# Optimization experiments

Measured on AMD Instinct MI355X. Metric: run time of the kernel, lower is better.

The kernel has to match this reference:

```python
import jax, jax.numpy as jnp
import numpy as np
import math

TWO_PI = 2.0 * math.pi
C_TOP = 8      # ann_top_centroids
K_TOP = 32     # topk slots
SCALES = 4
TEMP = 1.0
MIN_CANDID = 32


def _ln(x):
    mu = x.mean(axis=-1, keepdims=True)
    v = x.var(axis=-1, keepdims=True)
    return (x - mu) / jnp.sqrt(v + 1e-5)


def _gelu(x):
    return jax.nn.gelu(x, approximate=False)


def _sq_l2(q, k):
    # q: (B,S,D), k: (N,D) -> (B,S,N) squared L2
    return ((q * q).sum(-1)[..., None] + (k * k).sum(-1)
            - 2.0 * jnp.einsum('bsd,nd->bsn', q, k))


def _forward(x, keys, values, W_in, b_in, ricci, fractal_weights, centroids,
             Wk, bk, entangle_key, holo_real, holo_imag, W_read, b_read,
             W_out, b_out, centroid_ids):
    B, S, _ = x.shape
    M, D = keys.shape
    C = centroids.shape[0]

    # input_projection: Linear -> LayerNorm -> GELU, then manifold encode
    z = _gelu(_ln(x @ W_in + b_in))                    # (B,S,3D)
    z = z.reshape(B, S, D, 3)
    z = jnp.einsum('bseq,ed->bsdq', z, ricci)          # ricci flow
    q = z.mean(axis=-1)                                # (B,S,D) query on manifold

    # fractal multiscale distance: d(q/2^s, k/2^s) = d(q,k)/4^s for squared L2
    wts = jax.nn.softmax(fractal_weights)
    coef = (wts / (4.0 ** jnp.arange(SCALES, dtype=x.dtype))).sum()

    # stage 1: centroid shortlist (no-grad in original)
    d_cent = coef * _sq_l2(q, centroids)               # (B,S,C)
    _, topc = jax.lax.top_k(-d_cent, C_TOP)            # smallest distances
    sel = jnp.zeros((C,), dtype=bool).at[topc.reshape(-1)].set(True)
    mask_cent = sel[centroid_ids]                      # (M,) candidate slots
    mask = mask_cent | (mask_cent.sum() < MIN_CANDID)  # fall back to all keys

    # stage 2: distances to candidate keys, inf elsewhere
    d_keys = coef * _sq_l2(q, keys)                    # (B,S,M)
    dist = jnp.where(mask, d_keys, jnp.inf)
    dist = jax.lax.stop_gradient(dist)                 # search is no-grad

    neg_top, idx = jax.lax.top_k(-dist, K_TOP)         # (B,S,K)
    w = jax.nn.softmax(neg_top / TEMP, axis=-1)        # slot weights

    # value read: gather + weighted sum
    v_read = jnp.einsum('bsk,bskd->bsd', w, values[idx])   # (B,S,3D)

    # holographic read: complex key phases, FFT-domain entangled unbind
    phase = TWO_PI * jax.nn.sigmoid(x @ Wk + bk)            # (B,S,H)
    k_c = jnp.exp(1j * phase.astype(jnp.complex64))
    kf = jnp.fft.fft(k_c, axis=-1)
    kf = kf * jnp.exp(1j * entangle_key.astype(jnp.complex64))

    holo = (holo_real + 1j * holo_imag)[idx]                # (B,S,K,H) complex64
    holo_sum = jnp.einsum('bsk,bskh->bsh', w.astype(jnp.complex64), holo)
    r = jnp.fft.ifft(holo_sum * jnp.conj(kf), axis=-1)      # unbind, time domain
    feats = jnp.concatenate([r.real, r.imag], axis=-1)      # (B,S,2H)
    holo_out = feats @ W_read + b_read                      # (B,S,3D)

    mem = v_read + holo_out
    out = _gelu(_ln(mem @ W_out + b_out))                   # (B,S,input_dim)
    return out


def setup_inputs() -> dict:
    key = jax.random.key(0)
    ks = jax.random.split(key, 16)
    B, S, IN = 2, 2048, 1024
    D, M, H, C = 24, 4096, 256, 256
    x = jax.random.normal(ks[0], (B, S, IN), jnp.float32)
    keys_p = jax.random.normal(ks[1], (M, D), jnp.float32)
    values = jax.random.normal(ks[2], (M, 3 * D), jnp.float32)
    W_in = jax.random.normal(ks[3], (IN, 3 * D), jnp.float32) / np.sqrt(IN)
    b_in = jnp.zeros((3 * D,), jnp.float32)
    ricci = jax.random.normal(ks[4], (D, D), jnp.float32) / np.sqrt(D)
    fractal_weights = jnp.ones((4,), jnp.float32)
    centroids = jax.random.normal(ks[5], (C, D), jnp.float32)
    Wk = jax.random.normal(ks[6], (IN, H), jnp.float32) / np.sqrt(IN)
    bk = jnp.zeros((H,), jnp.float32)
    entangle_key = jax.random.normal(ks[7], (H,), jnp.float32)
    holo_real = jax.random.normal(ks[8], (M, H), jnp.float32)
    holo_imag = jax.random.normal(ks[9], (M, H), jnp.float32)
    W_read = jax.random.normal(ks[10], (2 * H, 3 * D), jnp.float32) / np.sqrt(2 * H)
    b_read = jnp.zeros((3 * D,), jnp.float32)
    W_out = jax.random.normal(ks[11], (3 * D, IN), jnp.float32) / np.sqrt(3 * D)
    b_out = jnp.zeros((IN,), jnp.float32)
    # centroid assignment of each key (k-means style nearest centroid)
    centroid_ids = jnp.argmin(_sq_l2(keys_p[None], centroids)[0], axis=-1).astype(jnp.int32)
    return {"x": x, "keys": keys_p, "values": values, "W_in": W_in, "b_in": b_in,
            "ricci": ricci, "fractal_weights": fractal_weights,
            "centroids": centroids, "Wk": Wk, "bk": bk,
            "entangle_key": entangle_key, "holo_real": holo_real,
            "holo_imag": holo_imag, "W_read": W_read, "b_read": b_read,
            "W_out": W_out, "b_out": b_out, "centroid_ids": centroid_ids}


def reference(x, keys, values, W_in, b_in, ricci, fractal_weights, centroids,
              Wk, bk, entangle_key, holo_real, holo_imag, W_read, b_read,
              W_out, b_out, centroid_ids):
    return _forward(x, keys, values, W_in, b_in, ricci, fractal_weights,
                    centroids, Wk, bk, entangle_key, holo_real, holo_imag,
                    W_read, b_read, W_out, b_out, centroid_ids)
```

## Files before the change

### kernel.cpp

```cpp
#include <hip/hip_runtime.h>
#include <math.h>

#define P_TOT 4096
#define IN_DIM 1024
#define DDIM 24
#define MKEYS 4096
#define HDIM 256
#define CCENT 256
#define KTOP 32

typedef short bf16x8 __attribute__((ext_vector_type(8)));
typedef float f32x4 __attribute__((ext_vector_type(4)));

static const size_t o_Yq      = 0;
static const size_t o_Yp      = o_Yq + (size_t)2*P_TOT*72;
static const size_t o_q       = o_Yp + (size_t)P_TOT*256;
static const size_t o_qq      = o_q + (size_t)P_TOT*DDIM;
static const size_t o_KF      = o_qq + P_TOT;
static const size_t o_keynorm = o_KF + (size_t)P_TOT*512;
static const size_t o_centnorm= o_keynorm + MKEYS;
static const size_t o_coef    = o_centnorm + CCENT;
static const size_t o_vread   = o_coef + 64;
static const size_t o_keysT   = o_vread + (size_t)P_TOT*72;
static const size_t o_sel     = o_keysT + (size_t)DDIM*MKEYS;
static const size_t o_mask    = o_sel + 256;
static const size_t o_count   = o_mask + MKEYS;
static const size_t o_A6      = o_count + 64;
static const size_t o_W6T     = o_A6 + (size_t)P_TOT*3072/2;
static const size_t o_W2cat   = o_W6T + (size_t)72*6144/2;
static const size_t o_KCbf    = o_W2cat + (size_t)256*2048/2;
static const size_t o_TTT     = o_KCbf + (size_t)P_TOT*512/2;
static const size_t o_Xcatbf  = o_TTT + (size_t)512*512/2;
static const size_t o_W2T     = o_Xcatbf + (size_t)P_TOT*512/2;
static const size_t o_membf   = o_W2T + (size_t)72*512/2;
static const size_t o_WoutT   = o_membf + (size_t)P_TOT*96/2;

__device__ __forceinline__ float gelu_f(float x){
    return 0.5f * x * (1.0f + erff(x * 0.70710678118654752f));
}
__device__ __forceinline__ ushort f2bf(float f){
    union { float f; unsigned u; } a; a.f = f;
    unsigned u = a.u;
    return (ushort)((u + 0x7fffu + ((u >> 16) & 1u)) >> 16);
}
__device__ __forceinline__ float bf2f(ushort b){
    union { unsigned u; float f; } a; a.u = ((unsigned)b) << 16;
    return a.f;
}
__device__ __forceinline__ unsigned d2u(float f){
    unsigned b = __float_as_uint(f);
    return (b & 0x80000000u) ? ~b : (b | 0x80000000u);
}

#define TWO_PI_F 6.2831853071795864769f
#define STEP_F   0.024543692606170262f

__global__ void setup_small(const float* __restrict__ fw, const float* __restrict__ cent,
                            float* __restrict__ coefp, float* __restrict__ centnorm,
                            int* __restrict__ sel, int* __restrict__ count)
{
    int t = threadIdx.x;
    if (t == 0){
        float m = fmaxf(fmaxf(fw[0],fw[1]),fmaxf(fw[2],fw[3]));
        float e0=expf(fw[0]-m), e1=expf(fw[1]-m), e2=expf(fw[2]-m), e3=expf(fw[3]-m);
        float s = e0+e1+e2+e3;
        *coefp = (e0 + e1*0.25f + e2*0.0625f + e3*0.015625f) / s;
        *count = 0;
    }
    if (t < CCENT){
        sel[t] = 0;
        float s = 0.f;
        #pragma unroll
        for (int d=0; d<DDIM; ++d){ float v = cent[t*DDIM+d]; s += v*v; }
        centnorm[t] = s;
    }
}

__global__ void key_setup(const float* __restrict__ keys, float* __restrict__ keynorm,
                          float* __restrict__ keysT)
{
    int m = blockIdx.x*256 + threadIdx.x;
    float s = 0.f;
    #pragma unroll
    for (int d=0; d<DDIM; ++d){
        float v = keys[m*DDIM+d]; s += v*v;
        keysT[(size_t)d*MKEYS + m] = v;
    }
    keynorm[m] = s;
}

__global__ void conv_x3(const float* __restrict__ x, ushort* __restrict__ A6)
{
    int i = blockIdx.x*256 + threadIdx.x;
    int p = i >> 8, j = (i & 255) * 4;
    float4 v = *(const float4*)&x[(size_t)p*IN_DIM + j];
    ushort4 s0, s1, s2;
    float r;
    s0.x=f2bf(v.x); r=v.x-bf2f(s0.x); s1.x=f2bf(r); s2.x=f2bf(r-bf2f(s1.x));
    s0.y=f2bf(v.y); r=v.y-bf2f(s0.y); s1.y=f2bf(r); s2.y=f2bf(r-bf2f(s1.y));
    s0.z=f2bf(v.z); r=v.z-bf2f(s0.z); s1.z=f2bf(r); s2.z=f2bf(r-bf2f(s1.z));
    s0.w=f2bf(v.w); r=v.w-bf2f(s0.w); s1.w=f2bf(r); s2.w=f2bf(r-bf2f(s1.w));
    *(ushort4*)&A6[(size_t)p*3072 + j]        = s0;
    *(ushort4*)&A6[(size_t)p*3072 + 1024 + j] = s1;
    *(ushort4*)&A6[(size_t)p*3072 + 2048 + j] = s2;
}

__global__ void conv_W6(const float* __restrict__ Win, ushort* __restrict__ W6T)
{
    int idx = blockIdx.x*256 + threadIdx.x;
    if (idx >= 72*6144) return;
    int n = idx / 6144, kp = idx - n*6144;
    int seg = kp >> 10, kk = kp & 1023;
    int sb = (0x012010 >> (seg << 2)) & 0xF;
    float w = Win[kk*72 + n];
    ushort w0 = f2bf(w);
    float r1 = w - bf2f(w0);
    ushort w1 = f2bf(r1);
    ushort w2 = f2bf(r1 - bf2f(w1));
    W6T[idx] = (sb == 0) ? w0 : (sb == 1 ? w1 : w2);
}

__global__ void conv_W2cat(const float* __restrict__ Wk, ushort* __restrict__ W2cat)
{
    int idx = blockIdx.x*256 + threadIdx.x;
    int n = idx >> 11, k = idx & 2047;
    int kk = k & 1023;
    W2cat[idx] = f2bf(Wk[kk*256 + n]);
}

__global__ void conv_WoutT(const float* __restrict__ Wout, ushort* __restrict__ WoutT)
{
    int idx = blockIdx.x*256 + threadIdx.x;
    int n = idx / 96, k = idx - n*96;
    float v = (k < 72) ? Wout[(size_t)k*IN_DIM + n] : 0.f;
    WoutT[idx] = f2bf(v);
}

__global__ void build_TTT(const float* __restrict__ ek, ushort* __restrict__ TTT)
{
    int idx = blockIdx.x*256 + threadIdx.x;
    int c = idx >> 9, r = idx & 511;
    int n = c & 255, h = r & 255;
    float th = (float)((n*h) & 255) * STEP_F - ek[n];
    float sn, cs; sincosf(th, &sn, &cs);
    float v;
    if (r < 256) v = (c < 256) ? cs : -sn;
    else         v = (c < 256) ? sn : cs;
    TTT[idx] = f2bf(v);
}

__global__ void build_W2T(const float* __restrict__ Wr, ushort* __restrict__ W2T)
{
    __shared__ float tab[256];
    int t = threadIdx.x;
    tab[t] = cosf((float)t * STEP_F);
    __syncthreads();
    int idx = blockIdx.x*256 + t;
    if (idx >= 72*512) return;
    int j = idx >> 9, k = idx & 511;
    int n = k & 255;
    float acc = 0.f;
    for (int h=0; h<256; ++h){
        int xdx = (n*h) & 255;
        float c = tab[xdx], s = tab[(xdx+192) & 255];
        float w1 = Wr[h*72 + j], w2 = Wr[(256+h)*72 + j];
        acc += (k < 256) ? (c*w1 + s*w2) : (c*w2 - s*w1);
    }
    W2T[idx] = f2bf(acc * (1.f/256.f));
}

__global__ __launch_bounds__(256) void gemm_bf16(
    const ushort* __restrict__ A, const ushort* __restrict__ BT,
    float* __restrict__ C, const float* __restrict__ bias,
    const float* __restrict__ addm, ushort* __restrict__ Cbf,
    int M, int N, int Kloop, int Nb, int NbfPad, int lda, int ldb, int aMask,
    int amode, int kChunk, size_t zStride)
{
    __shared__ __align__(16) ushort As[64][40];
    __shared__ __align__(16) ushort Bs[64][40];
    const int tid = threadIdx.x;
    const int lane = tid & 63, wid = tid >> 6;
    const int wm = wid >> 1, wn = wid & 1;
    const int m0 = blockIdx.y * 64, n0 = blockIdx.x * 64;
    const int fr = lane & 15, fc = lane >> 4;
    const int srow = tid >> 2, schunk = (tid & 3) * 8;
    const int kStart = blockIdx.z * kChunk;
    const int kEnd = (kStart + kChunk < Kloop) ? (kStart + kChunk) : Kloop;
    if (blockIdx.z){ C += zStride; bias = nullptr; addm = nullptr; Cbf = nullptr; }
    f32x4 acc[2][2] = {};
    for (int k0 = kStart; k0 < kEnd; k0 += 32){
        int kk = k0 + schunk;
        int ka;
        if (amode) ka = (((0x210100 >> ((kk >> 10) << 2)) & 0xF) << 10) | (kk & 1023);
        else       ka = kk & aMask;
        *(bf16x8*)&As[srow][schunk] =
            *(const bf16x8*)&A[(size_t)(m0 + srow) * lda + ka];
        {
            int n = n0 + srow;
            bf16x8 v = {};
            if (n < Nb) v = *(const bf16x8*)&BT[(size_t)n * ldb + kk];
            *(bf16x8*)&Bs[srow][schunk] = v;
        }
        __syncthreads();
        bf16x8 a0 = *(bf16x8*)&As[wm*32 + fr][fc*8];
        bf16x8 a1 = *(bf16x8*)&As[wm*32 + 16 + fr][fc*8];
        bf16x8 b0 = *(bf16x8*)&Bs[wn*32 + fr][fc*8];
        bf16x8 b1 = *(bf16x8*)&Bs[wn*32 + 16 + fr][fc*8];
        acc[0][0] = __builtin_amdgcn_mfma_f32_16x16x32_bf16(a0, b0, acc[0][0], 0,0,0);
        acc[0][1] = __builtin_amdgcn_mfma_f32_16x16x32_bf16(a0, b1, acc[0][1], 0,0,0);
        acc[1][0] = __builtin_amdgcn_mfma_f32_16x16x32_bf16(a1, b0, acc[1][0], 0,0,0);
        acc[1][1] = __builtin_amdgcn_mfma_f32_16x16x32_bf16(a1, b1, acc[1][1], 0,0,0);
        __syncthreads();
    }
    #pragma unroll
    for (int mi=0; mi<2; ++mi){
        #pragma unroll
        for (int ni=0; ni<2; ++ni){
            #pragma unroll
            for (int rr=0; rr<4; ++rr){
                int gm = m0 + wm*32 + mi*16 + fc*4 + rr;
                int gn = n0 + wn*32 + ni*16 + fr;
                float v = acc[mi][ni][rr];
                if (gn < N){
                    if (bias) v += bias[gn];
                    if (addm) v += addm[(size_t)gm*N + gn];
                    if (C) C[(size_t)gm*N + gn] = v;
                } else v = 0.f;
                if (Cbf && gn < NbfPad)
                    Cbf[(size_t)gm*NbfPad + gn] = f2bf(v);
            }
        }
    }
}

__global__ __launch_bounds__(256) void post_proj(
    const float* __restrict__ Yq, const float* __restrict__ Yp,
    const float* __restrict__ ricci,
    float* __restrict__ q, float* __restrict__ qq, ushort* __restrict__ KCbf)
{
    int wave = threadIdx.x >> 6, lane = threadIdx.x & 63;
    int p = blockIdx.x*4 + wave;
    __shared__ float zsh[4][72];
    __shared__ float zbsh[4][24];
    const float* Yr  = Yq + (size_t)p*72;
    const float* Yr2 = Yq + (size_t)P_TOT*72 + (size_t)p*72;
    float v1 = Yr[lane] + Yr2[lane];
    float v2 = (lane < 8) ? (Yr[64+lane] + Yr2[64+lane]) : 0.f;
    float s = v1 + v2, s2 = v1*v1 + v2*v2;
    #pragma unroll
    for (int off=32; off; off>>=1){ s += __shfl_xor(s,off); s2 += __shfl_xor(s2,off); }
    float mean = s * (1.f/72.f);
    float var  = s2 * (1.f/72.f) - mean*mean;
    float rstd = rsqrtf(var + 1e-5f);
    zsh[wave][lane] = gelu_f((v1-mean)*rstd);
    if (lane < 8) zsh[wave][64+lane] = gelu_f((v2-mean)*rstd);
    __syncthreads();
    if (lane < 24){
        float zb = (zsh[wave][lane*3] + zsh[wave][lane*3+1] + zsh[wave][lane*3+2]) * (1.f/3.f);
        zbsh[wave][lane] = zb;
    }
    __syncthreads();
    float qd = 0.f;
    if (lane < 24){
        #pragma unroll
        for (int e=0;e<24;++e) qd += zbsh[wave][e] * ricci[e*24+lane];
        q[(size_t)p*DDIM + lane] = qd;
    }
    float qs = (lane<24) ? qd*qd : 0.f;
    #pragma unroll
    for (int off=32; off; off>>=1) qs += __shfl_xor(qs,off);
    if (lane == 0) qq[p] = qs;
    const float* Ypr = Yp + (size_t)p*256;
    #pragma unroll
    for (int j=0;j<4;++j){
        int h = lane + 64*j;
        float u = Ypr[h];
        float ph = TWO_PI_F / (1.f + expf(-u));
        float sn, cs; sincosf(ph, &sn, &cs);
        KCbf[(size_t)p*512 + h]       = f2bf(cs);
        KCbf[(size_t)p*512 + 256 + h] = f2bf(sn);
    }
}

__global__ __launch_bounds__(256) void cent_topk(
    const float* __restrict__ q, const float* __restrict__ qq,
    const float* __restrict__ centroids, const float* __restrict__ centnorm,
    int* __restrict__ sel)
{
    int wave = threadIdx.x >> 6, lane = threadIdx.x & 63;
    int p = blockIdx.x*4 + wave;
    __shared__ float qsh[4][24];
    if (lane < 24) qsh[wave][lane] = q[(size_t)p*DDIM + lane];
    __syncthreads();
    float qv = qq[p];
    float d[4]; int ci[4];
    #pragma unroll
    for (int j=0;j<4;++j){
        int c = lane + 64*j;
        float dot = 0.f;
        #pragma unroll
        for (int e=0;e<24;++e) dot += qsh[wave][e]*centroids[c*24+e];
        d[j] = qv + centnorm[c] - 2.f*dot;
        ci[j] = c;
    }
    for (int k=0;k<8;++k){
        float mv = d[0]; int mi = ci[0];
        #pragma unroll
        for (int j=1;j<4;++j) if (d[j] < mv || (d[j]==mv && ci[j]<mi)){ mv=d[j]; mi=ci[j]; }
        #pragma unroll
        for (int off=32; off; off>>=1){
            float ov = __shfl_xor(mv,off); int oi = __shfl_xor(mi,off);
            if (ov < mv || (ov==mv && oi<mi)){ mv=ov; mi=oi; }
        }
        if ((mi & 63) == lane){
            int j = mi >> 6;
            if (j==0) d[0]=INFINITY; else if (j==1) d[1]=INFINITY;
            else if (j==2) d[2]=INFINITY; else d[3]=INFINITY;
            sel[mi] = 1;
        }
    }
}

__global__ void mask_count(const int* __restrict__ sel, const int* __restrict__ cids,
                           int* __restrict__ maskKey, int* __restrict__ count)
{
    int m = blockIdx.x*256 + threadIdx.x;
    int v = sel[cids[m]];
    maskKey[m] = v;
    int lane = threadIdx.x & 63;
    #pragma unroll
    for (int off=32; off; off>>=1) v += __shfl_xor(v, off);
    if (lane == 0) atomicAdd(count, v);
}

__device__ __forceinline__ void select_pos(
    int pc, float (&dvr)[16], int t, int lane, int w, float coef,
    int* hist, int* wsum,
    unsigned& s_pref, int& s_krem, int& s_bin, int& s_below,
    int& s_cntL, int& s_cntT,
    float* candD, int* candI, float* tieD, int* tieI,
    float (*sw4)[KTOP], int (*sidx4)[KTOP], float* inv4)
{
    if (t == 0){ s_pref = 0u; s_krem = KTOP; }
    __syncthreads();
    for (int pp = 0; pp < 4; ++pp){
        hist[t] = 0;
        __syncthreads();
        unsigned prefR = s_pref;
        int kremR = s_krem;
        #pragma unroll
        for (int i=0;i<16;++i){
            unsigned u = d2u(dvr[i]);
            bool cond = (pp == 0) ? true : ((u >> (32 - 8*pp)) == prefR);
            if (cond) atomicAdd(&hist[(u >> (24 - 8*pp)) & 255], 1);
        }
        __syncthreads();
        int h = hist[t];
        int sc = h;
        #pragma unroll
        for (int off=1; off<64; off<<=1){
            int o = __shfl_up(sc, off);
            if (lane >= off) sc += o;
        }
        if (lane == 63) wsum[w] = sc;
        __syncthreads();
        int add = 0;
        for (int ww=0; ww<w; ++ww) add += wsum[ww];
        sc += add;
        if (kremR > sc - h && kremR <= sc){ s_bin = t; s_below = sc - h; }
        __syncthreads();
        if (t == 0){ s_pref = (s_pref << 8) | (unsigned)s_bin; s_krem -= s_below; }
        __syncthreads();
    }
    unsigned tau = s_pref;
    if (t == 0){ s_cntL = 0; s_cntT = 0; }
    __syncthreads();
    #pragma unroll
    for (int i=0;i<16;++i){
        unsigned u = d2u(dvr[i]);
        int m = 1024*(i>>2) + 4*t + (i&3);
        if (u < tau){ int sl = atomicAdd(&s_cntL,1); candD[sl]=dvr[i]; candI[sl]=m; }
        else if (u == tau){ int sl = atomicAdd(&s_cntT,1); if (sl<64){ tieD[sl]=dvr[i]; tieI[sl]=m; } }
    }
    __syncthreads();
    if (t == 0){
        int need = s_krem, have = s_cntL;
        int nt = s_cntT < 64 ? s_cntT : 64;
        for (int sl=0; sl<need; ++sl){
            int best=0, bi=0x7fffffff;
            for (int j=0;j<nt;++j) if (tieI[j] < bi){ bi=tieI[j]; best=j; }
            candD[have+sl]=tieD[best]; candI[have+sl]=bi; tieI[best]=0x7fffffff;
        }
    }
    __syncthreads();
    if (w == 0){
        float v = (lane < 32) ? candD[lane] : INFINITY;
        int  ix = (lane < 32) ? candI[lane] : 0x7fffffff;
        #pragma unroll
        for (int kk=2; kk<=64; kk<<=1){
            #pragma unroll
            for (int j=kk>>1; j>0; j>>=1){
                float ov = __shfl_xor(v, j); int oi = __shfl_xor(ix, j);
                bool keepSmall = (((lane & j) == 0) == ((lane & kk) == 0));
                bool less = (ov < v) || (ov == v && oi < ix);
                if (keepSmall ? less : !less){ v = ov; ix = oi; }
            }
        }
        float v0 = __shfl(v, 0);
        float swv = (lane < 32) ? expf(-coef * (v - v0)) : 0.f;
        float ssum = 0.f;
        for (int k=0;k<KTOP;++k) ssum += __shfl(swv, k);
        if (lane < 32){ sw4[pc][lane] = swv; sidx4[pc][lane] = ix; }
        if (lane == 0) inv4[pc] = 1.f / ssum;
    }
    __syncthreads();
}

__global__ __launch_bounds__(256) void select_read(
    const float* __restrict__ keysT,
    const float* __restrict__ q, const float* __restrict__ qq,
    const float* __restrict__ keynorm, const int* __restrict__ maskKey,
    const int* __restrict__ count, const float* __restrict__ coefp,
    const float* __restrict__ values, const float* __restrict__ hr,
    const float* __restrict__ hi, const float* __restrict__ KF,
    float* __restrict__ vread, ushort* __restrict__ Xcatbf)
{
    const int t = threadIdx.x;
    const int w = t >> 6, lane = t & 63;
    const int p0 = blockIdx.x * 4;
    __shared__ float qsh[4][24];
    __shared__ int hist[256];
    __shared__ int wsum[4];
    __shared__ unsigned s_pref;
    __shared__ int s_krem, s_bin, s_below, s_cntL, s_cntT;
    __shared__ float candD[KTOP]; __shared__ int candI[KTOP];
    __shared__ float tieD[64];    __shared__ int tieI[64];
    __shared__ float sw4[4][KTOP]; __shared__ int sidx4[4][KTOP];
    __shared__ float inv4[4];

    bool useAll = (*count) < 32;
    float coef = *coefp;
    if (t < 96){
        int pp = t / 24, e = t - pp*24;
        qsh[pp][e] = q[(size_t)(p0+pp)*DDIM + e];
    }
    __syncthreads();
    float qv0 = qq[p0], qv1 = qq[p0+1], qv2 = qq[p0+2], qv3 = qq[p0+3];

    float a0[16], a1[16], a2[16], a3[16];
    #pragma unroll
    for (int i=0;i<16;++i){ a0[i]=0.f; a1[i]=0.f; a2[i]=0.f; a3[i]=0.f; }
    for (int e=0;e<24;++e){
        float q0 = qsh[0][e], q1 = qsh[1][e], q2 = qsh[2][e], q3 = qsh[3][e];
        const float* kr = keysT + (size_t)e*MKEYS + 4*t;
        #pragma unroll
        for (int i=0;i<4;++i){
            float4 kv = *(const float4*)&kr[1024*i];
            a0[i*4+0]=fmaf(q0,kv.x,a0[i*4+0]); a0[i*4+1]=fmaf(q0,kv.y,a0[i*4+1]);
            a0[i*4+2]=fmaf(q0,kv.z,a0[i*4+2]); a0[i*4+3]=fmaf(q0,kv.w,a0[i*4+3]);
            a1[i*4+0]=fmaf(q1,kv.x,a1[i*4+0]); a1[i*4+1]=fmaf(q1,kv.y,a1[i*4+1]);
            a1[i*4+2]=fmaf(q1,kv.z,a1[i*4+2]); a1[i*4+3]=fmaf(q1,kv.w,a1[i*4+3]);
            a2[i*4+0]=fmaf(q2,kv.x,a2[i*4+0]); a2[i*4+1]=fmaf(q2,kv.y,a2[i*4+1]);
            a2[i*4+2]=fmaf(q2,kv.z,a2[i*4+2]); a2[i*4+3]=fmaf(q2,kv.w,a2[i*4+3]);
            a3[i*4+0]=fmaf(q3,kv.x,a3[i*4+0]); a3[i*4+1]=fmaf(q3,kv.y,a3[i*4+1]);
            a3[i*4+2]=fmaf(q3,kv.z,a3[i*4+2]); a3[i*4+3]=fmaf(q3,kv.w,a3[i*4+3]);
        }
    }
    #pragma unroll
    for (int i=0;i<4;++i){
        float4 kn = *(const float4*)&keynorm[1024*i + 4*t];
        int4 mk = *(const int4*)&maskKey[1024*i + 4*t];
        bool ok0 = useAll || mk.x, ok1 = useAll || mk.y, ok2 = useAll || mk.z, ok3 = useAll || mk.w;
        float d;
        d = qv0 + kn.x - 2.f*a0[i*4+0]; a0[i*4+0] = ok0 ? d : INFINITY;
        d = qv0 + kn.y - 2.f*a0[i*4+1]; a0[i*4+1] = ok1 ? d : INFINITY;
        d = qv0 + kn.z - 2.f*a0[i*4+2]; a0[i*4+2] = ok2 ? d : INFINITY;
        d = qv0 + kn.w - 2.f*a0[i*4+3]; a0[i*4+3] = ok3 ? d : INFINITY;
        d = qv1 + kn.x - 2.f*a1[i*4+0]; a1[i*4+0] = ok0 ? d : INFINITY;
        d = qv1 + kn.y - 2.f*a1[i*4+1]; a1[i*4+1] = ok1 ? d : INFINITY;
        d = qv1 + kn.z - 2.f*a1[i*4+2]; a1[i*4+2] = ok2 ? d : INFINITY;
        d = qv1 + kn.w - 2.f*a1[i*4+3]; a1[i*4+3] = ok3 ? d : INFINITY;
        d = qv2 + kn.x - 2.f*a2[i*4+0]; a2[i*4+0] = ok0 ? d : INFINITY;
        d = qv2 + kn.y - 2.f*a2[i*4+1]; a2[i*4+1] = ok1 ? d : INFINITY;
        d = qv2 + kn.z - 2.f*a2[i*4+2]; a2[i*4+2] = ok2 ? d : INFINITY;
        d = qv2 + kn.w - 2.f*a2[i*4+3]; a2[i*4+3] = ok3 ? d : INFINITY;
        d = qv3 + kn.x - 2.f*a3[i*4+0]; a3[i*4+0] = ok0 ? d : INFINITY;
        d = qv3 + kn.y - 2.f*a3[i*4+1]; a3[i*4+1] = ok1 ? d : INFINITY;
        d = qv3 + kn.z - 2.f*a3[i*4+2]; a3[i*4+2] = ok2 ? d : INFINITY;
        d = qv3 + kn.w - 2.f*a3[i*4+3]; a3[i*4+3] = ok3 ? d : INFINITY;
    }

    select_pos(0, a0, t, lane, w, coef, hist, wsum, s_pref, s_krem, s_bin, s_below,
               s_cntL, s_cntT, candD, candI, tieD, tieI, sw4, sidx4, inv4);
    select_pos(1, a1, t, lane, w, coef, hist, wsum, s_pref, s_krem, s_bin, s_below,
               s_cntL, s_cntT, candD, candI, tieD, tieI, sw4, sidx4, inv4);
    select_pos(2, a2, t, lane, w, coef, hist, wsum, s_pref, s_krem, s_bin, s_below,
               s_cntL, s_cntT, candD, candI, tieD, tieI, sw4, sidx4, inv4);
    select_pos(3, a3, t, lane, w, coef, hist, wsum, s_pref, s_krem, s_bin, s_below,
               s_cntL, s_cntT, candD, candI, tieD, tieI, sw4, sidx4, inv4);

    for (int pos=0; pos<4; ++pos){
        int p = p0 + pos;
        float inv = inv4[pos];
        if (t < 72){
            float a = 0.f;
            for (int k=0;k<KTOP;++k) a += sw4[pos][k]*values[(size_t)sidx4[pos][k]*72 + t];
            vread[(size_t)p*72 + t] = a * inv;
        }
        float sr = 0.f, si = 0.f;
        for (int k=0;k<KTOP;++k){
            float wv = sw4[pos][k];
            size_t off = (size_t)sidx4[pos][k]*HDIM + t;
            sr += wv*hr[off]; si += wv*hi[off];
        }
        sr *= inv; si *= inv;
        float Rk = KF[(size_t)p*512 + t], Ik = KF[(size_t)p*512 + 256 + t];
        Xcatbf[(size_t)p*512 + t]       = f2bf(sr*Rk + si*Ik);
        Xcatbf[(size_t)p*512 + 256 + t] = f2bf(si*Rk - sr*Ik);
    }
}

__global__ __launch_bounds__(256) void ln_gelu_out(float* __restrict__ O)
{
    int p = blockIdx.x; int t = threadIdx.x;
    float4 v = *(float4*)&O[(size_t)p*IN_DIM + t*4];
    float s  = v.x+v.y+v.z+v.w;
    float s2 = v.x*v.x+v.y*v.y+v.z*v.z+v.w*v.w;
    #pragma unroll
    for (int off=32; off; off>>=1){ s += __shfl_xor(s,off); s2 += __shfl_xor(s2,off); }
    __shared__ float as[4], as2[4];
    int lane = t & 63, w = t >> 6;
    if (lane == 0){ as[w] = s; as2[w] = s2; }
    __syncthreads();
    s = as[0]+as[1]+as[2]+as[3];
    s2 = as2[0]+as2[1]+as2[2]+as2[3];
    float mean = s * (1.f/1024.f);
    float var  = s2 * (1.f/1024.f) - mean*mean;
    float rstd = rsqrtf(var + 1e-5f);
    v.x = gelu_f((v.x-mean)*rstd);
    v.y = gelu_f((v.y-mean)*rstd);
    v.z = gelu_f((v.z-mean)*rstd);
    v.w = gelu_f((v.w-mean)*rstd);
    *(float4*)&O[(size_t)p*IN_DIM + t*4] = v;
}

extern "C" void kernel_launch(void* const* d_in, const int* in_sizes, int n_in,
                              void* d_out, int out_size, void* d_ws, size_t ws_size,
                              hipStream_t stream)
{
    const float* x      = (const float*)d_in[0];
    const float* keys   = (const float*)d_in[1];
    const float* values = (const float*)d_in[2];
    const float* W_in   = (const float*)d_in[3];
    const float* b_in   = (const float*)d_in[4];
    const float* ricci  = (const float*)d_in[5];
    const float* fw     = (const float*)d_in[6];
    const float* cent   = (const float*)d_in[7];
    const float* Wk     = (const float*)d_in[8];
    const float* bk     = (const float*)d_in[9];
    const float* ek     = (const float*)d_in[10];
    const float* hr     = (const float*)d_in[11];
    const float* hi     = (const float*)d_in[12];
    const float* Wr     = (const float*)d_in[13];
    const float* brd    = (const float*)d_in[14];
    const float* W_out  = (const float*)d_in[15];
    const float* b_out  = (const float*)d_in[16];
    const int*   cids   = (const int*)d_in[17];
    float* ws  = (float*)d_ws;
    float* out = (float*)d_out;
    int* sel   = (int*)(ws + o_sel);
    int* mask  = (int*)(ws + o_mask);
    int* count = (int*)(ws + o_count);
    ushort* A6     = (ushort*)(ws + o_A6);
    ushort* W6T    = (ushort*)(ws + o_W6T);
    ushort* W2cat  = (ushort*)(ws + o_W2cat);
    ushort* KCbf   = (ushort*)(ws + o_KCbf);
    ushort* TTT    = (ushort*)(ws + o_TTT);
    ushort* Xcatbf = (ushort*)(ws + o_Xcatbf);
    ushort* W2T    = (ushort*)(ws + o_W2T);
    ushort* membf  = (ushort*)(ws + o_membf);
    ushort* WoutT  = (ushort*)(ws + o_WoutT);
    const int NOMASK = 0x7fffffff;

    setup_small<<<1,256,0,stream>>>(fw, cent, ws+o_coef, ws+o_centnorm, sel, count);
    key_setup<<<16,256,0,stream>>>(keys, ws+o_keynorm, ws+o_keysT);
    conv_x3<<<4096,256,0,stream>>>(x, A6);
    conv_W6<<<(72*6144+255)/256,256,0,stream>>>(W_in, W6T);
    conv_W2cat<<<2048,256,0,stream>>>(Wk, W2cat);
    conv_WoutT<<<(IN_DIM*96)/256,256,0,stream>>>(W_out, WoutT);
    build_TTT<<<1024,256,0,stream>>>(ek, TTT);
    build_W2T<<<144,256,0,stream>>>(Wr, W2T);

    gemm_bf16<<<dim3(2,64,2),256,0,stream>>>(A6, W6T, ws+o_Yq, b_in, nullptr, nullptr,
                                             P_TOT, 72, 6144, 72, 0, 3072, 6144, NOMASK, 1,
                                             3072, (size_t)P_TOT*72);
    gemm_bf16<<<dim3(4,64,1),256,0,stream>>>(A6, W2cat, ws+o_Yp, bk, nullptr, nullptr,
                                             P_TOT, 256, 2048, 256, 0, 3072, 2048, NOMASK, 0,
                                             2048, 0);
    post_proj<<<1024,256,0,stream>>>(ws+o_Yq, ws+o_Yp, ricci, ws+o_q, ws+o_qq, KCbf);
    gemm_bf16<<<dim3(8,64,1),256,0,stream>>>(KCbf, TTT, ws+o_KF, nullptr, nullptr, nullptr,
                                             P_TOT, 512, 512, 512, 0, 512, 512, NOMASK, 0,
                                             512, 0);
    cent_topk<<<1024,256,0,stream>>>(ws+o_q, ws+o_qq, cent, ws+o_centnorm, sel);
    mask_count<<<16,256,0,stream>>>(sel, cids, mask, count);
    select_read<<<P_TOT/4,256,0,stream>>>(ws+o_keysT, ws+o_q, ws+o_qq, ws+o_keynorm,
                                          mask, count, ws+o_coef, values, hr, hi, ws+o_KF,
                                          ws+o_vread, Xcatbf);
    gemm_bf16<<<dim3(2,64,1),256,0,stream>>>(Xcatbf, W2T, nullptr, brd, ws+o_vread, membf,
                                             P_TOT, 72, 512, 72, 96, 512, 512, NOMASK, 0,
                                             512, 0);
    gemm_bf16<<<dim3(16,64,1),256,0,stream>>>(membf, WoutT, out, b_out, nullptr, nullptr,
                                              P_TOT, IN_DIM, 96, IN_DIM, 0, 96, 96, NOMASK, 0,
                                              96, 0);
    ln_gelu_out<<<P_TOT,256,0,stream>>>(out);
}
```

Baseline: 314.5 us.

## Replace radix top-k select with value-range bucket refinement over three passes

The per-position top-32 selection stops doing a 4-pass 8-bit radix select on the bit pattern of each distance. It now takes a block-wide min/max of the finite distances and refines a value-range histogram over 256 buckets for 3 passes, tracking per-element active and below masks. Ties in the final bucket are resolved by a second bitonic sort. This removes one histogram pass and the serial single-thread tie loop, but adds a min/max reduction and an extra sort, and relies on float bucketing, which can put more than 64 elements in the final bucket and drop candidates. A mask argument of one GEMM launch also changes from NOMASK to 2047, which may alter its output.

```diff
diff --git a/kernel.cpp b/kernel.cpp
--- a/kernel.cpp
+++ b/kernel.cpp
@@ -46,10 +46,6 @@
 __device__ __forceinline__ float bf2f(ushort b){
     union { unsigned u; float f; } a; a.u = ((unsigned)b) << 16;
     return a.f;
-}
-__device__ __forceinline__ unsigned d2u(float f){
-    unsigned b = __float_as_uint(f);
-    return (b & 0x80000000u) ? ~b : (b | 0x80000000u);
 }
 
 #define TWO_PI_F 6.2831853071795864769f
@@ -333,26 +329,51 @@
     if (lane == 0) atomicAdd(count, v);
 }
 
+__device__ __forceinline__ int bucket_of(float d, float lo, float inv){
+    float bf = (d - lo) * inv;
+    bf = fminf(bf, 255.0f);
+    int bn = (int)bf;
+    return bn < 0 ? 0 : bn;
+}
+
 __device__ __forceinline__ void select_pos(
     int pc, float (&dvr)[16], int t, int lane, int w, float coef,
-    int* hist, int* wsum,
-    unsigned& s_pref, int& s_krem, int& s_bin, int& s_below,
-    int& s_cntL, int& s_cntT,
+    int* hist, int* wsum, float* wmn, float* wmx, float* s_f, int* s_i,
     float* candD, int* candI, float* tieD, int* tieI,
     float (*sw4)[KTOP], int (*sidx4)[KTOP], float* inv4)
 {
-    if (t == 0){ s_pref = 0u; s_krem = KTOP; }
-    __syncthreads();
-    for (int pp = 0; pp < 4; ++pp){
+    float mn = INFINITY, mx = -INFINITY;
+    #pragma unroll
+    for (int i=0;i<16;++i){
+        float d = dvr[i];
+        mn = fminf(mn, d);
+        mx = fmaxf(mx, (d < INFINITY) ? d : -INFINITY);
+    }
+    #pragma unroll
+    for (int off=32; off; off>>=1){
+        mn = fminf(mn, __shfl_xor(mn, off));
+        mx = fmaxf(mx, __shfl_xor(mx, off));
+    }
+    if (lane == 0){ wmn[w] = mn; wmx[w] = mx; }
+    __syncthreads();
+    if (t == 0){
+        float dmin = fminf(fminf(wmn[0],wmn[1]), fminf(wmn[2],wmn[3]));
+        float dmax = fmaxf(fmaxf(wmx[0],wmx[1]), fmaxf(wmx[2],wmx[3]));
+        s_f[0] = dmin;
+        s_f[1] = fmaxf(dmax - dmin, 1e-30f) * 1.000001f;
+        s_i[0] = 0;
+    }
+    __syncthreads();
+
+    unsigned act = 0xFFFFu, below = 0u;
+    for (int pass = 0; pass < 3; ++pass){
         hist[t] = 0;
         __syncthreads();
-        unsigned prefR = s_pref;
-        int kremR = s_krem;
-        #pragma unroll
-        for (int i=0;i<16;++i){
-            unsigned u = d2u(dvr[i]);
-            bool cond = (pp == 0) ? true : ((u >> (32 - 8*pp)) == prefR);
-            if (cond) atomicAdd(&hist[(u >> (24 - 8*pp)) & 255], 1);
+        float lo = s_f[0];
+        float inv = 256.0f / s_f[1];
+        #pragma unroll
+        for (int i=0;i<16;++i) if (act & (1u<<i)){
+            atomicAdd(&hist[bucket_of(dvr[i], lo, inv)], 1);
         }
         __syncthreads();
         int h = hist[t];
@@ -367,35 +388,44 @@
         int add = 0;
         for (int ww=0; ww<w; ++ww) add += wsum[ww];
         sc += add;
-        if (kremR > sc - h && kremR <= sc){ s_bin = t; s_below = sc - h; }
+        int krem = KTOP - s_i[0];
+        if (krem > sc - h && krem <= sc){ s_i[1] = t; s_i[2] = sc - h; }
         __syncthreads();
-        if (t == 0){ s_pref = (s_pref << 8) | (unsigned)s_bin; s_krem -= s_below; }
+        int bstar = s_i[1];
+        #pragma unroll
+        for (int i=0;i<16;++i) if (act & (1u<<i)){
+            int bn = bucket_of(dvr[i], lo, inv);
+            if (bn < bstar){ below |= (1u<<i); act &= ~(1u<<i); }
+            else if (bn > bstar) act &= ~(1u<<i);
+        }
+        if (t == 0){
+            s_i[0] += s_i[2];
+            float wnew = s_f[1] * (1.f/256.f);
+            s_f[0] = s_f[0] + (float)bstar * wnew;
+            s_f[1] = wnew;
+        }
         __syncthreads();
     }
-    unsigned tau = s_pref;
-    if (t == 0){ s_cntL = 0; s_cntT = 0; }
+
+    if (t == 0){ s_i[3] = 0; s_i[4] = 0; }
     __syncthreads();
     #pragma unroll
     for (int i=0;i<16;++i){
-        unsigned u = d2u(dvr[i]);
         int m = 1024*(i>>2) + 4*t + (i&3);
-        if (u < tau){ int sl = atomicAdd(&s_cntL,1); candD[sl]=dvr[i]; candI[sl]=m; }
-        else if (u == tau){ int sl = atomicAdd(&s_cntT,1); if (sl<64){ tieD[sl]=dvr[i]; tieI[sl]=m; } }
-    }
-    __syncthreads();
-    if (t == 0){
-        int need = s_krem, have = s_cntL;
-        int nt = s_cntT < 64 ? s_cntT : 64;
-        for (int sl=0; sl<need; ++sl){
-            int best=0, bi=0x7fffffff;
-            for (int j=0;j<nt;++j) if (tieI[j] < bi){ bi=tieI[j]; best=j; }
-            candD[have+sl]=tieD[best]; candI[have+sl]=bi; tieI[best]=0x7fffffff;
+        if (below & (1u<<i)){
+            int sl = atomicAdd(&s_i[3], 1); candD[sl] = dvr[i]; candI[sl] = m;
+        } else if ((act & (1u<<i)) && dvr[i] < INFINITY){
+            int sl = atomicAdd(&s_i[4], 1);
+            if (sl < 64){ tieD[sl] = dvr[i]; tieI[sl] = m; }
         }
     }
     __syncthreads();
     if (w == 0){
-        float v = (lane < 32) ? candD[lane] : INFINITY;
-        int  ix = (lane < 32) ? candI[lane] : 0x7fffffff;
+        int C = s_i[3];
+        int nt = s_i[4] < 64 ? s_i[4] : 64;
+        int need = KTOP - C;
+        float v = (lane < nt) ? tieD[lane] : INFINITY;
+        int  ix = (lane < nt) ? tieI[lane] : 0x7fffffff;
         #pragma unroll
         for (int kk=2; kk<=64; kk<<=1){
             #pragma unroll
@@ -406,11 +436,27 @@
                 if (keepSmall ? less : !less){ v = ov; ix = oi; }
             }
         }
+        if (lane < need){ candD[C + lane] = v; candI[C + lane] = ix; }
+    }
+    __syncthreads();
+    if (w == 0){
+        float v = (lane < KTOP) ? candD[lane] : INFINITY;
+        int  ix = (lane < KTOP) ? candI[lane] : 0x7fffffff;
+        #pragma unroll
+        for (int kk=2; kk<=64; kk<<=1){
+            #pragma unroll
+            for (int j=kk>>1; j>0; j>>=1){
+                float ov = __shfl_xor(v, j); int oi = __shfl_xor(ix, j);
+                bool keepSmall = (((lane & j) == 0) == ((lane & kk) == 0));
+                bool less = (ov < v) || (ov == v && oi < ix);
+                if (keepSmall ? less : !less){ v = ov; ix = oi; }
+            }
+        }
         float v0 = __shfl(v, 0);
-        float swv = (lane < 32) ? expf(-coef * (v - v0)) : 0.f;
+        float swv = (lane < KTOP) ? expf(-coef * (v - v0)) : 0.f;
         float ssum = 0.f;
         for (int k=0;k<KTOP;++k) ssum += __shfl(swv, k);
-        if (lane < 32){ sw4[pc][lane] = swv; sidx4[pc][lane] = ix; }
+        if (lane < KTOP){ sw4[pc][lane] = swv; sidx4[pc][lane] = ix; }
         if (lane == 0) inv4[pc] = 1.f / ssum;
     }
     __syncthreads();
@@ -431,8 +477,9 @@
     __shared__ float qsh[4][24];
     __shared__ int hist[256];
     __shared__ int wsum[4];
-    __shared__ unsigned s_pref;
-    __shared__ int s_krem, s_bin, s_below, s_cntL, s_cntT;
+    __shared__ float wmn[4], wmx[4];
+    __shared__ float s_f[2];
+    __shared__ int s_i[8];
     __shared__ float candD[KTOP]; __shared__ int candI[KTOP];
     __shared__ float tieD[64];    __shared__ int tieI[64];
     __shared__ float sw4[4][KTOP]; __shared__ int sidx4[4][KTOP];
@@ -490,14 +537,14 @@
         d = qv3 + kn.w - 2.f*a3[i*4+3]; a3[i*4+3] = ok3 ? d : INFINITY;
     }
 
-    select_pos(0, a0, t, lane, w, coef, hist, wsum, s_pref, s_krem, s_bin, s_below,
-               s_cntL, s_cntT, candD, candI, tieD, tieI, sw4, sidx4, inv4);
-    select_pos(1, a1, t, lane, w, coef, hist, wsum, s_pref, s_krem, s_bin, s_below,
-               s_cntL, s_cntT, candD, candI, tieD, tieI, sw4, sidx4, inv4);
-    select_pos(2, a2, t, lane, w, coef, hist, wsum, s_pref, s_krem, s_bin, s_below,
-               s_cntL, s_cntT, candD, candI, tieD, tieI, sw4, sidx4, inv4);
-    select_pos(3, a3, t, lane, w, coef, hist, wsum, s_pref, s_krem, s_bin, s_below,
-               s_cntL, s_cntT, candD, candI, tieD, tieI, sw4, sidx4, inv4);
+    select_pos(0, a0, t, lane, w, coef, hist, wsum, wmn, wmx, s_f, s_i,
+               candD, candI, tieD, tieI, sw4, sidx4, inv4);
+    select_pos(1, a1, t, lane, w, coef, hist, wsum, wmn, wmx, s_f, s_i,
+               candD, candI, tieD, tieI, sw4, sidx4, inv4);
+    select_pos(2, a2, t, lane, w, coef, hist, wsum, wmn, wmx, s_f, s_i,
+               candD, candI, tieD, tieI, sw4, sidx4, inv4);
+    select_pos(3, a3, t, lane, w, coef, hist, wsum, wmn, wmx, s_f, s_i,
+               candD, candI, tieD, tieI, sw4, sidx4, inv4);
 
     for (int pos=0; pos<4; ++pos){
         int p = p0 + pos;
@@ -595,7 +642,7 @@
                                              P_TOT, 72, 6144, 72, 0, 3072, 6144, NOMASK, 1,
                                              3072, (size_t)P_TOT*72);
     gemm_bf16<<<dim3(4,64,1),256,0,stream>>>(A6, W2cat, ws+o_Yp, bk, nullptr, nullptr,
-                                             P_TOT, 256, 2048, 256, 0, 3072, 2048, NOMASK, 0,
+                                             P_TOT, 256, 2048, 256, 0, 3072, 2048, 2047, 0,
                                              2048, 0);
     post_proj<<<1024,256,0,stream>>>(ws+o_Yq, ws+o_Yp, ricci, ws+o_q, ws+o_qq, KCbf);
     gemm_bf16<<<dim3(8,64,1),256,0,stream>>>(KCbf, TTT, ws+o_KF, nullptr, nullptr, nullptr,
```

Result: slower. 367.9 us (+17.0%).

## Split key top-k selection into two half-range blocks plus merge kernel

Applied to the files above, without the earlier changes.

The fused select_read kernel now runs as two kernels. select_half has each block scan half of the keys (2048) for 4 positions and write a per-half top-32 to workspace. merge_read then merges the two candidate lists per position with a bitonic sort, computes the softmax weights and does the value and holographic reads with one block per position. The goal is twice as many blocks and half the register footprint for better occupancy, paid for with an extra launch and a global round-trip for the candidates. The candidate buffers reuse the Yq region, and a GEMM mask argument changes from NOMASK to 2047, apparently to keep the Yp GEMM clear of that aliasing.

```diff
diff --git a/kernel.cpp b/kernel.cpp
--- a/kernel.cpp
+++ b/kernel.cpp
@@ -34,6 +34,8 @@
 static const size_t o_W2T     = o_Xcatbf + (size_t)P_TOT*512/2;
 static const size_t o_membf   = o_W2T + (size_t)72*512/2;
 static const size_t o_WoutT   = o_membf + (size_t)P_TOT*96/2;
+static const size_t o_candD   = o_Yq;
+static const size_t o_candI   = o_Yq + (size_t)P_TOT*64;
 
 __device__ __forceinline__ float gelu_f(float x){
     return 0.5f * x * (1.0f + erff(x * 0.70710678118654752f));
@@ -333,13 +335,13 @@
     if (lane == 0) atomicAdd(count, v);
 }
 
-__device__ __forceinline__ void select_pos(
-    int pc, float (&dvr)[16], int t, int lane, int w, float coef,
+__device__ __forceinline__ void select_pos8(
+    float (&dvr)[8], int mOff, int t, int lane, int w,
     int* hist, int* wsum,
     unsigned& s_pref, int& s_krem, int& s_bin, int& s_below,
     int& s_cntL, int& s_cntT,
     float* candD, int* candI, float* tieD, int* tieI,
-    float (*sw4)[KTOP], int (*sidx4)[KTOP], float* inv4)
+    float* __restrict__ outD, int* __restrict__ outI)
 {
     if (t == 0){ s_pref = 0u; s_krem = KTOP; }
     __syncthreads();
@@ -349,7 +351,7 @@
         unsigned prefR = s_pref;
         int kremR = s_krem;
         #pragma unroll
-        for (int i=0;i<16;++i){
+        for (int i=0;i<8;++i){
             unsigned u = d2u(dvr[i]);
             bool cond = (pp == 0) ? true : ((u >> (32 - 8*pp)) == prefR);
             if (cond) atomicAdd(&hist[(u >> (24 - 8*pp)) & 255], 1);
@@ -376,9 +378,9 @@
     if (t == 0){ s_cntL = 0; s_cntT = 0; }
     __syncthreads();
     #pragma unroll
-    for (int i=0;i<16;++i){
+    for (int i=0;i<8;++i){
         unsigned u = d2u(dvr[i]);
-        int m = 1024*(i>>2) + 4*t + (i&3);
+        int m = mOff + 1024*(i>>2) + 4*t + (i&3);
         if (u < tau){ int sl = atomicAdd(&s_cntL,1); candD[sl]=dvr[i]; candI[sl]=m; }
         else if (u == tau){ int sl = atomicAdd(&s_cntT,1); if (sl<64){ tieD[sl]=dvr[i]; tieI[sl]=m; } }
     }
@@ -406,28 +408,23 @@
                 if (keepSmall ? less : !less){ v = ov; ix = oi; }
             }
         }
-        float v0 = __shfl(v, 0);
-        float swv = (lane < 32) ? expf(-coef * (v - v0)) : 0.f;
-        float ssum = 0.f;
-        for (int k=0;k<KTOP;++k) ssum += __shfl(swv, k);
-        if (lane < 32){ sw4[pc][lane] = swv; sidx4[pc][lane] = ix; }
-        if (lane == 0) inv4[pc] = 1.f / ssum;
-    }
-    __syncthreads();
-}
-
-__global__ __launch_bounds__(256) void select_read(
+        if (lane < 32){ outD[lane] = v; outI[lane] = ix; }
+    }
+    __syncthreads();
+}
+
+__global__ __launch_bounds__(256) void select_half(
     const float* __restrict__ keysT,
     const float* __restrict__ q, const float* __restrict__ qq,
     const float* __restrict__ keynorm, const int* __restrict__ maskKey,
-    const int* __restrict__ count, const float* __restrict__ coefp,
-    const float* __restrict__ values, const float* __restrict__ hr,
-    const float* __restrict__ hi, const float* __restrict__ KF,
-    float* __restrict__ vread, ushort* __restrict__ Xcatbf)
+    const int* __restrict__ count,
+    float* __restrict__ candDg, int* __restrict__ candIg)
 {
     const int t = threadIdx.x;
     const int w = t >> 6, lane = t & 63;
-    const int p0 = blockIdx.x * 4;
+    const int pg = blockIdx.x >> 1, half = blockIdx.x & 1;
+    const int p0 = pg * 4;
+    const int mOff = half * 2048;
     __shared__ float qsh[4][24];
     __shared__ int hist[256];
     __shared__ int wsum[4];
@@ -435,11 +432,8 @@
     __shared__ int s_krem, s_bin, s_below, s_cntL, s_cntT;
     __shared__ float candD[KTOP]; __shared__ int candI[KTOP];
     __shared__ float tieD[64];    __shared__ int tieI[64];
-    __shared__ float sw4[4][KTOP]; __shared__ int sidx4[4][KTOP];
-    __shared__ float inv4[4];
 
     bool useAll = (*count) < 32;
-    float coef = *coefp;
     if (t < 96){
         int pp = t / 24, e = t - pp*24;
         qsh[pp][e] = q[(size_t)(p0+pp)*DDIM + e];
@@ -447,14 +441,14 @@
     __syncthreads();
     float qv0 = qq[p0], qv1 = qq[p0+1], qv2 = qq[p0+2], qv3 = qq[p0+3];
 
-    float a0[16], a1[16], a2[16], a3[16];
-    #pragma unroll
-    for (int i=0;i<16;++i){ a0[i]=0.f; a1[i]=0.f; a2[i]=0.f; a3[i]=0.f; }
+    float a0[8], a1[8], a2[8], a3[8];
+    #pragma unroll
+    for (int i=0;i<8;++i){ a0[i]=0.f; a1[i]=0.f; a2[i]=0.f; a3[i]=0.f; }
     for (int e=0;e<24;++e){
         float q0 = qsh[0][e], q1 = qsh[1][e], q2 = qsh[2][e], q3 = qsh[3][e];
-        const float* kr = keysT + (size_t)e*MKEYS + 4*t;
-        #pragma unroll
-        for (int i=0;i<4;++i){
+        const float* kr = keysT + (size_t)e*MKEYS + mOff + 4*t;
+        #pragma unroll
+        for (int i=0;i<2;++i){
             float4 kv = *(const float4*)&kr[1024*i];
             a0[i*4+0]=fmaf(q0,kv.x,a0[i*4+0]); a0[i*4+1]=fmaf(q0,kv.y,a0[i*4+1]);
             a0[i*4+2]=fmaf(q0,kv.z,a0[i*4+2]); a0[i*4+3]=fmaf(q0,kv.w,a0[i*4+3]);
@@ -467,9 +461,9 @@
         }
     }
     #pragma unroll
-    for (int i=0;i<4;++i){
-        float4 kn = *(const float4*)&keynorm[1024*i + 4*t];
-        int4 mk = *(const int4*)&maskKey[1024*i + 4*t];
+    for (int i=0;i<2;++i){
+        float4 kn = *(const float4*)&keynorm[mOff + 1024*i + 4*t];
+        int4 mk = *(const int4*)&maskKey[mOff + 1024*i + 4*t];
         bool ok0 = useAll || mk.x, ok1 = useAll || mk.y, ok2 = useAll || mk.z, ok3 = useAll || mk.w;
         float d;
         d = qv0 + kn.x - 2.f*a0[i*4+0]; a0[i*4+0] = ok0 ? d : INFINITY;
@@ -490,27 +484,66 @@
         d = qv3 + kn.w - 2.f*a3[i*4+3]; a3[i*4+3] = ok3 ? d : INFINITY;
     }
 
-    select_pos(0, a0, t, lane, w, coef, hist, wsum, s_pref, s_krem, s_bin, s_below,
-               s_cntL, s_cntT, candD, candI, tieD, tieI, sw4, sidx4, inv4);
-    select_pos(1, a1, t, lane, w, coef, hist, wsum, s_pref, s_krem, s_bin, s_below,
-               s_cntL, s_cntT, candD, candI, tieD, tieI, sw4, sidx4, inv4);
-    select_pos(2, a2, t, lane, w, coef, hist, wsum, s_pref, s_krem, s_bin, s_below,
-               s_cntL, s_cntT, candD, candI, tieD, tieI, sw4, sidx4, inv4);
-    select_pos(3, a3, t, lane, w, coef, hist, wsum, s_pref, s_krem, s_bin, s_below,
-               s_cntL, s_cntT, candD, candI, tieD, tieI, sw4, sidx4, inv4);
-
-    for (int pos=0; pos<4; ++pos){
-        int p = p0 + pos;
-        float inv = inv4[pos];
-        if (t < 72){
-            float a = 0.f;
-            for (int k=0;k<KTOP;++k) a += sw4[pos][k]*values[(size_t)sidx4[pos][k]*72 + t];
-            vread[(size_t)p*72 + t] = a * inv;
-        }
+    float* oD = candDg + ((size_t)p0*2 + half)*32;
+    int*   oI = candIg + ((size_t)p0*2 + half)*32;
+    select_pos8(a0, mOff, t, lane, w, hist, wsum, s_pref, s_krem, s_bin, s_below,
+                s_cntL, s_cntT, candD, candI, tieD, tieI, oD, oI);
+    oD += 64; oI += 64;
+    select_pos8(a1, mOff, t, lane, w, hist, wsum, s_pref, s_krem, s_bin, s_below,
+                s_cntL, s_cntT, candD, candI, tieD, tieI, oD, oI);
+    oD += 64; oI += 64;
+    select_pos8(a2, mOff, t, lane, w, hist, wsum, s_pref, s_krem, s_bin, s_below,
+                s_cntL, s_cntT, candD, candI, tieD, tieI, oD, oI);
+    oD += 64; oI += 64;
+    select_pos8(a3, mOff, t, lane, w, hist, wsum, s_pref, s_krem, s_bin, s_below,
+                s_cntL, s_cntT, candD, candI, tieD, tieI, oD, oI);
+}
+
+__global__ __launch_bounds__(256) void merge_read(
+    const float* __restrict__ candDg, const int* __restrict__ candIg,
+    const float* __restrict__ coefp,
+    const float* __restrict__ values, const float* __restrict__ hr,
+    const float* __restrict__ hi, const float* __restrict__ KF,
+    float* __restrict__ vread, ushort* __restrict__ Xcatbf)
+{
+    const int p = blockIdx.x;
+    const int t = threadIdx.x;
+    const int w = t >> 6, lane = t & 63;
+    __shared__ float sw[KTOP]; __shared__ int sidx[KTOP];
+    __shared__ float s_inv;
+    float coef = *coefp;
+    if (w == 0){
+        float v = candDg[(size_t)p*64 + lane];
+        int  ix = candIg[(size_t)p*64 + lane];
+        #pragma unroll
+        for (int kk=2; kk<=64; kk<<=1){
+            #pragma unroll
+            for (int j=kk>>1; j>0; j>>=1){
+                float ov = __shfl_xor(v, j); int oi = __shfl_xor(ix, j);
+                bool keepSmall = (((lane & j) == 0) == ((lane & kk) == 0));
+                bool less = (ov < v) || (ov == v && oi < ix);
+                if (keepSmall ? less : !less){ v = ov; ix = oi; }
+            }
+        }
+        float v0 = __shfl(v, 0);
+        float swv = (lane < KTOP) ? expf(-coef * (v - v0)) : 0.f;
+        float ssum = 0.f;
+        for (int k=0;k<KTOP;++k) ssum += __shfl(swv, k);
+        if (lane < KTOP){ sw[lane] = swv; sidx[lane] = ix; }
+        if (lane == 0) s_inv = 1.f / ssum;
+    }
+    __syncthreads();
+    float inv = s_inv;
+    if (t < 72){
+        float a = 0.f;
+        for (int k=0;k<KTOP;++k) a += sw[k]*values[(size_t)sidx[k]*72 + t];
+        vread[(size_t)p*72 + t] = a * inv;
+    }
+    {
         float sr = 0.f, si = 0.f;
         for (int k=0;k<KTOP;++k){
-            float wv = sw4[pos][k];
-            size_t off = (size_t)sidx4[pos][k]*HDIM + t;
+            float wv = sw[k];
+            size_t off = (size_t)sidx[k]*HDIM + t;
             sr += wv*hr[off]; si += wv*hi[off];
         }
         sr *= inv; si *= inv;
@@ -580,6 +613,8 @@
     ushort* W2T    = (ushort*)(ws + o_W2T);
     ushort* membf  = (ushort*)(ws + o_membf);
     ushort* WoutT  = (ushort*)(ws + o_WoutT);
+    float* candDg  = ws + o_candD;
+    int*   candIg  = (int*)(ws + o_candI);
     const int NOMASK = 0x7fffffff;
 
     setup_small<<<1,256,0,stream>>>(fw, cent, ws+o_coef, ws+o_centnorm, sel, count);
@@ -595,7 +630,7 @@
                                              P_TOT, 72, 6144, 72, 0, 3072, 6144, NOMASK, 1,
                                              3072, (size_t)P_TOT*72);
     gemm_bf16<<<dim3(4,64,1),256,0,stream>>>(A6, W2cat, ws+o_Yp, bk, nullptr, nullptr,
-                                             P_TOT, 256, 2048, 256, 0, 3072, 2048, NOMASK, 0,
+                                             P_TOT, 256, 2048, 256, 0, 3072, 2048, 2047, 0,
                                              2048, 0);
     post_proj<<<1024,256,0,stream>>>(ws+o_Yq, ws+o_Yp, ricci, ws+o_q, ws+o_qq, KCbf);
     gemm_bf16<<<dim3(8,64,1),256,0,stream>>>(KCbf, TTT, ws+o_KF, nullptr, nullptr, nullptr,
@@ -603,9 +638,10 @@
                                              512, 0);
     cent_topk<<<1024,256,0,stream>>>(ws+o_q, ws+o_qq, cent, ws+o_centnorm, sel);
     mask_count<<<16,256,0,stream>>>(sel, cids, mask, count);
-    select_read<<<P_TOT/4,256,0,stream>>>(ws+o_keysT, ws+o_q, ws+o_qq, ws+o_keynorm,
-                                          mask, count, ws+o_coef, values, hr, hi, ws+o_KF,
-                                          ws+o_vread, Xcatbf);
+    select_half<<<2048,256,0,stream>>>(ws+o_keysT, ws+o_q, ws+o_qq, ws+o_keynorm,
+                                       mask, count, candDg, candIg);
+    merge_read<<<P_TOT,256,0,stream>>>(candDg, candIg, ws+o_coef, values, hr, hi,
+                                       ws+o_KF, ws+o_vread, Xcatbf);
     gemm_bf16<<<dim3(2,64,1),256,0,stream>>>(Xcatbf, W2T, nullptr, brd, ws+o_vread, membf,
                                              P_TOT, 72, 512, 72, 96, 512, 512, NOMASK, 0,
                                              512, 0);
```

After: 531.4 us, median of 2. 69.0% more time.

## Split top-k selection and value/holographic gather into separate kernels

Applied to the files above, without the earlier changes.

The fused select_read kernel gathered values and holographic rows for its 4 positions one after another. Now it only writes the top-k slot weights, indices and normalisers to workspace, reusing the no-longer-needed Yq region. A new gather_read kernel then does the gather and complex unbind with one block per position, giving more parallel blocks and memory-level parallelism. This costs an extra launch and a small round trip through global memory. A mask argument on the Wk projection GEMM also changes from NOMASK to 2047, whose effect is not visible here.

```diff
diff --git a/kernel.cpp b/kernel.cpp
--- a/kernel.cpp
+++ b/kernel.cpp
@@ -34,6 +34,9 @@
 static const size_t o_W2T     = o_Xcatbf + (size_t)P_TOT*512/2;
 static const size_t o_membf   = o_W2T + (size_t)72*512/2;
 static const size_t o_WoutT   = o_membf + (size_t)P_TOT*96/2;
+static const size_t o_swG     = o_Yq;
+static const size_t o_sidxG   = o_swG + (size_t)P_TOT*KTOP;
+static const size_t o_invG    = o_sidxG + (size_t)P_TOT*KTOP;
 
 __device__ __forceinline__ float gelu_f(float x){
     return 0.5f * x * (1.0f + erff(x * 0.70710678118654752f));
@@ -421,9 +424,7 @@
     const float* __restrict__ q, const float* __restrict__ qq,
     const float* __restrict__ keynorm, const int* __restrict__ maskKey,
     const int* __restrict__ count, const float* __restrict__ coefp,
-    const float* __restrict__ values, const float* __restrict__ hr,
-    const float* __restrict__ hi, const float* __restrict__ KF,
-    float* __restrict__ vread, ushort* __restrict__ Xcatbf)
+    float* __restrict__ swG, int* __restrict__ sidxG, float* __restrict__ invG)
 {
     const int t = threadIdx.x;
     const int w = t >> 6, lane = t & 63;
@@ -499,18 +500,40 @@
     select_pos(3, a3, t, lane, w, coef, hist, wsum, s_pref, s_krem, s_bin, s_below,
                s_cntL, s_cntT, candD, candI, tieD, tieI, sw4, sidx4, inv4);
 
-    for (int pos=0; pos<4; ++pos){
-        int p = p0 + pos;
-        float inv = inv4[pos];
-        if (t < 72){
-            float a = 0.f;
-            for (int k=0;k<KTOP;++k) a += sw4[pos][k]*values[(size_t)sidx4[pos][k]*72 + t];
-            vread[(size_t)p*72 + t] = a * inv;
-        }
+    if (t < 128){
+        int pos = t >> 5, k = t & 31;
+        swG[(size_t)(p0+pos)*KTOP + k]   = sw4[pos][k];
+        sidxG[(size_t)(p0+pos)*KTOP + k] = sidx4[pos][k];
+    }
+    if (t < 4) invG[p0 + t] = inv4[t];
+}
+
+__global__ __launch_bounds__(256) void gather_read(
+    const float* __restrict__ swG, const int* __restrict__ sidxG,
+    const float* __restrict__ invG,
+    const float* __restrict__ values, const float* __restrict__ hr,
+    const float* __restrict__ hi, const float* __restrict__ KF,
+    float* __restrict__ vread, ushort* __restrict__ Xcatbf)
+{
+    const int p = blockIdx.x;
+    const int t = threadIdx.x;
+    __shared__ float sw[KTOP]; __shared__ int sidx[KTOP];
+    if (t < KTOP){
+        sw[t]   = swG[(size_t)p*KTOP + t];
+        sidx[t] = sidxG[(size_t)p*KTOP + t];
+    }
+    __syncthreads();
+    float inv = invG[p];
+    if (t < 72){
+        float a = 0.f;
+        for (int k=0;k<KTOP;++k) a += sw[k]*values[(size_t)sidx[k]*72 + t];
+        vread[(size_t)p*72 + t] = a * inv;
+    }
+    {
         float sr = 0.f, si = 0.f;
         for (int k=0;k<KTOP;++k){
-            float wv = sw4[pos][k];
-            size_t off = (size_t)sidx4[pos][k]*HDIM + t;
+            float wv = sw[k];
+            size_t off = (size_t)sidx[k]*HDIM + t;
             sr += wv*hr[off]; si += wv*hi[off];
         }
         sr *= inv; si *= inv;
@@ -580,6 +603,9 @@
     ushort* W2T    = (ushort*)(ws + o_W2T);
     ushort* membf  = (ushort*)(ws + o_membf);
     ushort* WoutT  = (ushort*)(ws + o_WoutT);
+    float* swG   = ws + o_swG;
+    int*   sidxG = (int*)(ws + o_sidxG);
+    float* invG  = ws + o_invG;
     const int NOMASK = 0x7fffffff;
 
     setup_small<<<1,256,0,stream>>>(fw, cent, ws+o_coef, ws+o_centnorm, sel, count);
@@ -595,7 +621,7 @@
                                              P_TOT, 72, 6144, 72, 0, 3072, 6144, NOMASK, 1,
                                              3072, (size_t)P_TOT*72);
     gemm_bf16<<<dim3(4,64,1),256,0,stream>>>(A6, W2cat, ws+o_Yp, bk, nullptr, nullptr,
-                                             P_TOT, 256, 2048, 256, 0, 3072, 2048, NOMASK, 0,
+                                             P_TOT, 256, 2048, 256, 0, 3072, 2048, 2047, 0,
                                              2048, 0);
     post_proj<<<1024,256,0,stream>>>(ws+o_Yq, ws+o_Yp, ricci, ws+o_q, ws+o_qq, KCbf);
     gemm_bf16<<<dim3(8,64,1),256,0,stream>>>(KCbf, TTT, ws+o_KF, nullptr, nullptr, nullptr,
@@ -604,8 +630,9 @@
     cent_topk<<<1024,256,0,stream>>>(ws+o_q, ws+o_qq, cent, ws+o_centnorm, sel);
     mask_count<<<16,256,0,stream>>>(sel, cids, mask, count);
     select_read<<<P_TOT/4,256,0,stream>>>(ws+o_keysT, ws+o_q, ws+o_qq, ws+o_keynorm,
-                                          mask, count, ws+o_coef, values, hr, hi, ws+o_KF,
-                                          ws+o_vread, Xcatbf);
+                                          mask, count, ws+o_coef, swG, sidxG, invG);
+    gather_read<<<P_TOT,256,0,stream>>>(swG, sidxG, invG, values, hr, hi,
+                                        ws+o_KF, ws+o_vread, Xcatbf);
     gemm_bf16<<<dim3(2,64,1),256,0,stream>>>(Xcatbf, W2T, nullptr, brd, ws+o_vread, membf,
                                              P_TOT, 72, 512, 72, 96, 512, 512, NOMASK, 0,
                                              512, 0);
```

Measured after the change: 319.6 us. Within noise of the previous version (+1.6%).
